# Kernel tuning notes

Measured on AMD Instinct MI355X. Metric: run time of the kernel, lower is better.

Reference implementation:

```python
import jax, jax.numpy as jnp
import numpy as np

B, NUM_SLOTS, D, TOP_K = 2048, 128, 1024, 8
DH = D // 2  # route_mlp hidden


def setup_inputs() -> dict:
    key = jax.random.key(0)
    ks = jax.random.split(key, 16)
    s = 0.02
    return {
        "x": jax.random.normal(ks[0], (B, D), jnp.float32),
        "S": jax.random.normal(ks[1], (B, NUM_SLOTS, D), jnp.float32),
        # route_mlp: Linear(2D, D//2) -> GELU -> Linear(D//2, NUM_SLOTS)
        "w1": jax.random.normal(ks[2], (DH, 2 * D), jnp.float32) * s,
        "b1": jnp.zeros((DH,), jnp.float32),
        "w2": jax.random.normal(ks[3], (NUM_SLOTS, DH), jnp.float32) * s,
        "b2": jnp.zeros((NUM_SLOTS,), jnp.float32),
        # GRUCell(D, D): torch layout, gates ordered (r, z, n)
        "gru_wih": jax.random.normal(ks[4], (3 * D, D), jnp.float32) * s,
        "gru_whh": jax.random.normal(ks[5], (3 * D, D), jnp.float32) * s,
        "gru_bih": jnp.zeros((3 * D,), jnp.float32),
        "gru_bhh": jnp.zeros((3 * D,), jnp.float32),
        "wval": jax.random.normal(ks[6], (D, D), jnp.float32) * s,
        "bval": jnp.zeros((D,), jnp.float32),
        "wout": jax.random.normal(ks[7], (D, D), jnp.float32) * s,
        "bout": jnp.zeros((D,), jnp.float32),
        "tau": jnp.ones((1,), jnp.float32),
    }


def reference(x, S, w1, b1, w2, b2, gru_wih, gru_whh, gru_bih, gru_bhh,
              wval, bval, wout, bout, tau):
    # Routing: context = [x, mean over slots]
    slot_mean = S.mean(axis=1)                                  # [B, D]
    ctx = jnp.concatenate([x, slot_mean], axis=-1)              # [B, 2D]
    h = jax.nn.gelu(ctx @ w1.T + b1, approximate=False)         # [B, DH]
    route_logits = (h @ w2.T + b2) / (jnp.abs(tau) + 0.1)       # [B, NUM_SLOTS]

    topk_vals, topk_idx = jax.lax.top_k(route_logits, TOP_K)    # [B, K]
    topk_w = jax.nn.softmax(topk_vals, axis=-1)                 # [B, K]

    # Gather selected slot states
    slot_states = jnp.take_along_axis(S, topk_idx[:, :, None], axis=1)  # [B, K, D]

    # GRUCell (torch semantics). Input part shared across the K slots.
    gi = x @ gru_wih.T + gru_bih                                # [B, 3D]
    gh = slot_states @ gru_whh.T + gru_bhh                      # [B, K, 3D]
    gi_r, gi_z, gi_n = jnp.split(gi, 3, axis=-1)
    gh_r, gh_z, gh_n = jnp.split(gh, 3, axis=-1)
    r = jax.nn.sigmoid(gi_r[:, None, :] + gh_r)
    z = jax.nn.sigmoid(gi_z[:, None, :] + gh_z)
    n = jnp.tanh(gi_n[:, None, :] + r * gh_n)
    updated = (1.0 - z) * n + z * slot_states                   # [B, K, D]

    # Scatter updated states back into slot memory
    S_new = S.at[jnp.arange(B)[:, None], topk_idx].set(updated)

    # Weighted value readout
    values = updated @ wval.T + bval                            # [B, K, D]
    mixed = jnp.einsum('bkd,bk->bd', values, topk_w)            # [B, D]
    output = mixed @ wout.T + bout                              # [B, D]
    return output, S_new
```

## Files before the change

kernel.cpp:

```cpp
#include <hip/hip_runtime.h>
#include <math.h>
#include <stdint.h>

#define B_   2048
#define NS_  128
#define D_   1024
#define K_   8
#define DH_  512
#define G3_  3072

typedef unsigned short u16;
typedef short bf16x8 __attribute__((ext_vector_type(8)));
typedef float f32x4 __attribute__((ext_vector_type(4)));

__device__ __forceinline__ float bf2f(u16 u) {
  union { unsigned i; float f; } v; v.i = ((unsigned)u) << 16; return v.f;
}
__device__ __forceinline__ u16 f2bf(float f) {
  unsigned x = __float_as_uint(f);
  return (u16)((x + 0x7fffu + ((x >> 16) & 1u)) >> 16);
}

#define AS1C(p) ((const __attribute__((address_space(1))) void*)(uintptr_t)(p))
#define AS3(p)  ((__attribute__((address_space(3))) void*)(unsigned)(uintptr_t)(p))

template<int DO_COPY>
__global__ __launch_bounds__(256)
void sp_copymean(const float* __restrict__ S, float* __restrict__ Snew,
                 float* __restrict__ mean) {
  const int b = blockIdx.x;
  const int t = threadIdx.x, d0 = t * 4;
  const f32x4* src = (const f32x4*)(S + (size_t)b * NS_ * D_) + t;
  f32x4* dst = (f32x4*)(Snew + (size_t)b * NS_ * D_) + t;
  double a0 = 0, a1 = 0, a2 = 0, a3 = 0;
  #pragma unroll 4
  for (int s = 0; s < NS_; ++s) {
    f32x4 v = __builtin_nontemporal_load(src);
    if (DO_COPY) __builtin_nontemporal_store(v, dst);
    a0 += v[0]; a1 += v[1]; a2 += v[2]; a3 += v[3];
    src += 256; dst += 256;
  }
  float4 m;
  m.x = (float)(a0 * (1.0 / 128.0)); m.y = (float)(a1 * (1.0 / 128.0));
  m.z = (float)(a2 * (1.0 / 128.0)); m.w = (float)(a3 * (1.0 / 128.0));
  *(float4*)&mean[(size_t)b * D_ + d0] = m;
}

__global__ __launch_bounds__(256)
void sp_convert_all(const float* __restrict__ x, const float* __restrict__ wih,
                    const float* __restrict__ whh, const float* __restrict__ wval,
                    const float* __restrict__ wout,
                    u16* __restrict__ xb, u16* __restrict__ wihb,
                    u16* __restrict__ whhb, u16* __restrict__ wvalb,
                    u16* __restrict__ woutb) {
  const int stride = gridDim.x * 256;
  for (int i = blockIdx.x * 256 + threadIdx.x; i < 2621440; i += stride) {
    const float* s; u16* d; int off;
    if (i < 524288)       { s = x;    d = xb;    off = i; }
    else if (i < 1310720) { s = wih;  d = wihb;  off = i - 524288; }
    else if (i < 2097152) { s = whh;  d = whhb;  off = i - 1310720; }
    else if (i < 2359296) { s = wval; d = wvalb; off = i - 2097152; }
    else                  { s = wout; d = woutb; off = i - 2359296; }
    float4 v = ((const float4*)s)[off];
    ushort4 o;
    o.x = f2bf(v.x); o.y = f2bf(v.y); o.z = f2bf(v.z); o.w = f2bf(v.w);
    ((ushort4*)d)[off] = o;
  }
}

__global__ __launch_bounds__(256)
void sp_gemm1(const float* __restrict__ x, const float* __restrict__ mean,
              const float* __restrict__ w1, const float* __restrict__ bias1,
              float* __restrict__ h) {
  __shared__ float As[16][68];
  __shared__ float Bs[16][36];
  int wg = blockIdx.x;
  wg = (wg & 7) * 64 + (wg >> 3);
  const int n0 = (wg & 15) * 32;
  const int m0 = (wg >> 4) * 64;
  const int t = threadIdx.x;
  const int tx = t & 15, ty = t >> 4;
  float acc[4][2] = {};
  const int sr = t >> 2, sc = (t & 3) * 4;
  for (int k0 = 0; k0 < 2 * D_; k0 += 16) {
    const float* src = (k0 < D_) ? (x + k0) : (mean + (k0 - D_));
    float4 va = *(const float4*)&src[(size_t)(m0 + sr) * D_ + sc];
    As[sc + 0][sr] = va.x; As[sc + 1][sr] = va.y; As[sc + 2][sr] = va.z; As[sc + 3][sr] = va.w;
    if (t < 128) {
      const int bn = t >> 2, bc = (t & 3) * 4;
      float4 vb = *(const float4*)&w1[(size_t)(n0 + bn) * (2 * D_) + k0 + bc];
      Bs[bc + 0][bn] = vb.x; Bs[bc + 1][bn] = vb.y; Bs[bc + 2][bn] = vb.z; Bs[bc + 3][bn] = vb.w;
    }
    __syncthreads();
    #pragma unroll
    for (int kk = 0; kk < 16; ++kk) {
      float4 a = *(const float4*)&As[kk][ty * 4];
      float2 bb = *(const float2*)&Bs[kk][tx * 2];
      acc[0][0] = fmaf(a.x, bb.x, acc[0][0]); acc[0][1] = fmaf(a.x, bb.y, acc[0][1]);
      acc[1][0] = fmaf(a.y, bb.x, acc[1][0]); acc[1][1] = fmaf(a.y, bb.y, acc[1][1]);
      acc[2][0] = fmaf(a.z, bb.x, acc[2][0]); acc[2][1] = fmaf(a.z, bb.y, acc[2][1]);
      acc[3][0] = fmaf(a.w, bb.x, acc[3][0]); acc[3][1] = fmaf(a.w, bb.y, acc[3][1]);
    }
    __syncthreads();
  }
  #pragma unroll
  for (int i = 0; i < 4; ++i) {
    #pragma unroll
    for (int j = 0; j < 2; ++j) {
      const int r = m0 + ty * 4 + i, c = n0 + tx * 2 + j;
      float v = acc[i][j] + bias1[c];
      v = 0.5f * v * (1.0f + erff(v * 0.70710678118654752f));
      h[(size_t)r * DH_ + c] = v;
    }
  }
}

__global__ __launch_bounds__(64)
void sp_route_topk(const float* __restrict__ h, const float* __restrict__ w2,
                   const float* __restrict__ b2, const float* __restrict__ tau,
                   int* __restrict__ tki, float* __restrict__ tkw) {
  __shared__ float hs[DH_];
  const int b = blockIdx.x, l = threadIdx.x;
  *(float4*)&hs[l * 4] = *(const float4*)&h[(size_t)b * DH_ + l * 4];
  *(float4*)&hs[256 + l * 4] = *(const float4*)&h[(size_t)b * DH_ + 256 + l * 4];
  __syncthreads();
  const double invd = 1.0 / ((double)fabsf(tau[0]) + 0.1);
  float v[2]; int id[2];
  #pragma unroll
  for (int c = 0; c < 2; ++c) {
    const int n = c * 64 + l;
    const float* wr = &w2[(size_t)n * DH_];
    double s = 0.0;
    for (int j = 0; j < DH_; j += 4) {
      float4 w4 = *(const float4*)&wr[j];
      s += (double)hs[j] * (double)w4.x;
      s += (double)hs[j + 1] * (double)w4.y;
      s += (double)hs[j + 2] * (double)w4.z;
      s += (double)hs[j + 3] * (double)w4.w;
    }
    v[c] = (float)((s + (double)b2[n]) * invd);
    id[c] = n;
  }
  float m0f = 0.f, sum = 0.f, mye = 0.f; int myi = 0;
  for (int r = 0; r < 8; ++r) {
    float mv; int mi;
    if (v[1] > v[0]) { mv = v[1]; mi = id[1]; } else { mv = v[0]; mi = id[0]; }
    #pragma unroll
    for (int off = 32; off > 0; off >>= 1) {
      float ov = __shfl_xor(mv, off);
      int oi = __shfl_xor(mi, off);
      if (ov > mv || (ov == mv && oi < mi)) { mv = ov; mi = oi; }
    }
    if (r == 0) m0f = mv;
    float er = expf(mv - m0f);
    sum += er;
    if (l == r) { mye = er; myi = mi; }
    if (mi == id[0]) v[0] = -3.0e38f;
    if (mi == id[1]) v[1] = -3.0e38f;
  }
  if (l < 8) { tki[b * K_ + l] = myi; tkw[b * K_ + l] = mye / sum; }
}

__global__ __launch_bounds__(256)
void sp_gather(const float* __restrict__ S, const int* __restrict__ tki,
               u16* __restrict__ slotb) {
  const int blk = blockIdx.x;
  const int b = blk >> 3, k = blk & 7;
  const int s = tki[b * K_ + k];
  const int t = threadIdx.x;
  float4 v = *(const float4*)&S[((size_t)b * NS_ + s) * D_ + t * 4];
  ushort4 o;
  o.x = f2bf(v.x); o.y = f2bf(v.y); o.z = f2bf(v.z); o.w = f2bf(v.w);
  *(ushort4*)&slotb[((size_t)b * K_ + k) * D_ + t * 4] = o;
}

template<int EPI>
__global__ __launch_bounds__(256)
void sp_gemm_bf16(const u16* __restrict__ A, const u16* __restrict__ Bm,
                  void* __restrict__ Cv, const float* __restrict__ bias,
                  int M, int N, int Kd, int nbx) {
  __shared__ u16 lA[128 * 32];
  __shared__ u16 lB[128 * 32];
  int wg = blockIdx.x;
  {
    const int nwg = nbx * ((M + 127) >> 7);
    const int cpx = nwg >> 3;
    wg = (wg & 7) * cpx + (wg >> 3);
  }
  const int m0 = (wg / nbx) * 128, n0 = (wg % nbx) * 128;
  const int t = threadIdx.x;
  const int lane = t & 63;
  const int w = t >> 6;
  const int wm = w >> 1, wn = w & 1;

  f32x4 acc[4][4] = {};

  const int srow = t >> 2;
  const int scol = (t & 3) * 8;
  const u16* gA0 = A + (size_t)(m0 + srow) * Kd + scol;
  const u16* gA1 = A + (size_t)(m0 + 64 + srow) * Kd + scol;
  const u16* gB0 = Bm + (size_t)(n0 + srow) * Kd + scol;
  const u16* gB1 = Bm + (size_t)(n0 + 64 + srow) * Kd + scol;
  u16* lAw = &lA[(t & 192) * 8];
  u16* lBw = &lB[(t & 192) * 8];

  const int kb = (lane >> 4) * 8;
  const int rA = wm * 64 + (lane & 15);
  const int rB = wn * 64 + (lane & 15);

  for (int k0 = 0; k0 < Kd; k0 += 32) {
    __builtin_amdgcn_global_load_lds(AS1C(gA0 + k0), AS3(lAw), 16, 0, 0);
    __builtin_amdgcn_global_load_lds(AS1C(gA1 + k0), AS3(lAw + 2048), 16, 0, 0);
    __builtin_amdgcn_global_load_lds(AS1C(gB0 + k0), AS3(lBw), 16, 0, 0);
    __builtin_amdgcn_global_load_lds(AS1C(gB1 + k0), AS3(lBw + 2048), 16, 0, 0);
    __syncthreads();
    bf16x8 af[4], bfr[4];
    #pragma unroll
    for (int fm = 0; fm < 4; ++fm)
      af[fm] = *(const bf16x8*)&lA[(rA + fm * 16) * 32 + kb];
    #pragma unroll
    for (int fn = 0; fn < 4; ++fn)
      bfr[fn] = *(const bf16x8*)&lB[(rB + fn * 16) * 32 + kb];
    #pragma unroll
    for (int fm = 0; fm < 4; ++fm) {
      #pragma unroll
      for (int fn = 0; fn < 4; ++fn)
        acc[fm][fn] = __builtin_amdgcn_mfma_f32_16x16x32_bf16(af[fm], bfr[fn], acc[fm][fn], 0, 0, 0);
    }
    __syncthreads();
  }

  #pragma unroll
  for (int fm = 0; fm < 4; ++fm) {
    #pragma unroll
    for (int fn = 0; fn < 4; ++fn) {
      #pragma unroll
      for (int i = 0; i < 4; ++i) {
        const int r = m0 + wm * 64 + fm * 16 + (lane >> 4) * 4 + i;
        const int c = n0 + wn * 64 + fn * 16 + (lane & 15);
        float v = acc[fm][fn][i];
        if constexpr (EPI >= 2) v += bias[c];
        if constexpr (EPI == 0 || EPI == 2)
          ((float*)Cv)[(size_t)r * N + c] = v;
        else
          ((u16*)Cv)[(size_t)r * N + c] = f2bf(v);
      }
    }
  }
}

template<bool DIRECT>
__global__ __launch_bounds__(256)
void sp_gh_gru(const u16* __restrict__ slotb, const u16* __restrict__ whhb,
               const float* __restrict__ gi, const float* __restrict__ bih,
               const float* __restrict__ bhh, const int* __restrict__ tki,
               const float* __restrict__ tkw, float* __restrict__ dst,
               u16* __restrict__ umixb) {
  __shared__ u16 lA[64 * 32];
  __shared__ u16 lB[192 * 32];
  __shared__ int   sTki[64];
  __shared__ float sTkw[64];
  int wg = blockIdx.x;
  wg = (wg & 7) * 512 + (wg >> 3);
  const int mt = wg >> 4, db = wg & 15;
  const int m0 = mt * 64, d0 = db * 64;
  const int t = threadIdx.x;
  const int lane = t & 63, w = t >> 6;
  const int wm = w >> 1, wn = w & 1;
  const int lane15 = lane & 15, hi = lane >> 4;

  if (t < 64) { sTki[t] = tki[m0 + t]; sTkw[t] = tkw[m0 + t]; }

  f32x4 acc[2][6] = {};

  const int srow = t >> 2;
  const int scol = (t & 3) * 8;
  const u16* gA  = slotb + (size_t)(m0 + srow) * D_ + scol;
  const u16* gB0 = whhb + (size_t)(d0 + srow) * D_ + scol;
  const u16* gB1 = whhb + (size_t)(D_ + d0 + srow) * D_ + scol;
  const u16* gB2 = whhb + (size_t)(2 * D_ + d0 + srow) * D_ + scol;
  u16* lAw  = &lA[(t & 192) * 8];
  u16* lBw0 = &lB[(t & 192) * 8];

  const int kb = hi * 8;
  const int rA = wm * 32 + lane15;
  const int rB = wn * 32 + lane15;

  for (int k0 = 0; k0 < D_; k0 += 32) {
    __builtin_amdgcn_global_load_lds(AS1C(gA  + k0), AS3(lAw), 16, 0, 0);
    __builtin_amdgcn_global_load_lds(AS1C(gB0 + k0), AS3(lBw0), 16, 0, 0);
    __builtin_amdgcn_global_load_lds(AS1C(gB1 + k0), AS3(lBw0 + 2048), 16, 0, 0);
    __builtin_amdgcn_global_load_lds(AS1C(gB2 + k0), AS3(lBw0 + 4096), 16, 0, 0);
    __syncthreads();
    bf16x8 af[2], bfr[6];
    #pragma unroll
    for (int fm = 0; fm < 2; ++fm)
      af[fm] = *(const bf16x8*)&lA[(rA + fm * 16) * 32 + kb];
    #pragma unroll
    for (int g = 0; g < 3; ++g) {
      #pragma unroll
      for (int f = 0; f < 2; ++f)
        bfr[g * 2 + f] = *(const bf16x8*)&lB[(g * 64 + rB + f * 16) * 32 + kb];
    }
    #pragma unroll
    for (int fm = 0; fm < 2; ++fm) {
      #pragma unroll
      for (int fn = 0; fn < 6; ++fn)
        acc[fm][fn] = __builtin_amdgcn_mfma_f32_16x16x32_bf16(af[fm], bfr[fn], acc[fm][fn], 0, 0, 0);
    }
    __syncthreads();
  }

  #pragma unroll
  for (int fm = 0; fm < 2; ++fm) {
    const int rbase = wm * 32 + fm * 16 + hi * 4;
    const int bglob = (m0 + rbase) >> 3;
    #pragma unroll
    for (int f = 0; f < 2; ++f) {
      const int dg = d0 + wn * 32 + f * 16 + lane15;
      const float Gr = gi[(size_t)bglob * G3_ + dg]           + bih[dg];
      const float Gz = gi[(size_t)bglob * G3_ + D_ + dg]      + bih[D_ + dg];
      const float Gn = gi[(size_t)bglob * G3_ + 2 * D_ + dg]  + bih[2 * D_ + dg];
      const float Br = bhh[dg], Bz = bhh[D_ + dg], Bn = bhh[2 * D_ + dg];
      float part = 0.f;
      #pragma unroll
      for (int i = 0; i < 4; ++i) {
        const int row = rbase + i;
        const int grow = m0 + row;
        const float slot = bf2f(slotb[(size_t)grow * D_ + dg]);
        const float rr = acc[fm][f][i] + Br;
        const float zz = acc[fm][f + 2][i] + Bz;
        const float nn = acc[fm][f + 4][i] + Bn;
        const float rg = 1.f / (1.f + expf(-(Gr + rr)));
        const float zg = 1.f / (1.f + expf(-(Gz + zz)));
        const float ng = tanhf(Gn + rg * nn);
        const float uv = (1.f - zg) * ng + zg * slot;
        part = fmaf(sTkw[row], uv, part);
        if (DIRECT)
          dst[((size_t)bglob * NS_ + sTki[row]) * D_ + dg] = uv;
        else
          dst[(size_t)grow * D_ + dg] = uv;
      }
      part += __shfl_xor(part, 16);
      if ((hi & 1) == 0)
        umixb[(size_t)bglob * D_ + dg] = f2bf(part);
    }
  }
}

__global__ __launch_bounds__(256)
void sp_copy_scatter(const float* __restrict__ S, const float* __restrict__ upd,
                     const int* __restrict__ tki, float* __restrict__ Snew) {
  const int b = blockIdx.x, t = threadIdx.x;
  const int d0 = t * 4;
  int idx[K_];
  #pragma unroll
  for (int k = 0; k < K_; ++k) idx[k] = tki[b * K_ + k];
  for (int s = 0; s < NS_; ++s) {
    int sk = -1;
    #pragma unroll
    for (int k = 0; k < K_; ++k) if (idx[k] == s) sk = k;
    float4 v;
    if (sk >= 0) v = *(const float4*)&upd[((size_t)b * K_ + sk) * D_ + d0];
    else         v = *(const float4*)&S[((size_t)b * NS_ + s) * D_ + d0];
    *(float4*)&Snew[((size_t)b * NS_ + s) * D_ + d0] = v;
  }
}

extern "C" void kernel_launch(void* const* d_in, const int* in_sizes, int n_in,
                              void* d_out, int out_size, void* d_ws, size_t ws_size,
                              hipStream_t stream) {
  const float* x    = (const float*)d_in[0];
  const float* S    = (const float*)d_in[1];
  const float* w1   = (const float*)d_in[2];
  const float* b1   = (const float*)d_in[3];
  const float* w2   = (const float*)d_in[4];
  const float* b2   = (const float*)d_in[5];
  const float* wih  = (const float*)d_in[6];
  const float* whh  = (const float*)d_in[7];
  const float* bih  = (const float*)d_in[8];
  const float* bhh  = (const float*)d_in[9];
  const float* wval = (const float*)d_in[10];
  const float* bval = (const float*)d_in[11];
  const float* wout = (const float*)d_in[12];
  const float* bout = (const float*)d_in[13];
  const float* tau  = (const float*)d_in[14];

  float* out  = (float*)d_out;
  float* Snew = out + (size_t)B_ * D_;

  const bool bigws = ws_size >= (size_t)400 * 1024 * 1024;
  char* bigbase = bigws ? (char*)d_ws : (char*)Snew;
  size_t bo = 0;
  auto balloc = [&](size_t bytes) -> void* {
    void* p = bigbase + bo; bo += (bytes + 255) & ~(size_t)255; return p;
  };

  float* mean  = (float*)balloc((size_t)B_ * D_ * 4);
  float* h     = (float*)balloc((size_t)B_ * DH_ * 4);
  u16* xb      = (u16*)balloc((size_t)B_ * D_ * 2);
  u16* wihb    = (u16*)balloc((size_t)G3_ * D_ * 2);
  u16* whhb    = (u16*)balloc((size_t)G3_ * D_ * 2);
  u16* wvalb   = (u16*)balloc((size_t)D_ * D_ * 2);
  u16* woutb   = (u16*)balloc((size_t)D_ * D_ * 2);
  float* gi    = (float*)balloc((size_t)B_ * G3_ * 4);
  u16* slotb   = (u16*)balloc((size_t)B_ * K_ * D_ * 2);
  u16* umixb   = (u16*)balloc((size_t)B_ * D_ * 2);
  u16* mixedb  = (u16*)balloc((size_t)B_ * D_ * 2);

  char* wsb = (char*)d_ws;
  size_t so = bigws ? bo : 0;
  auto salloc = [&](size_t bytes) -> void* {
    void* p = wsb + so; so += (bytes + 255) & ~(size_t)255; return p;
  };
  int*   tki = (int*)salloc((size_t)B_ * K_ * 4);
  float* tkw = (float*)salloc((size_t)B_ * K_ * 4);
  float* upd = bigws ? nullptr : (float*)salloc((size_t)B_ * K_ * D_ * 4);

  if (bigws) sp_copymean<1><<<B_, 256, 0, stream>>>(S, Snew, mean);
  else       sp_copymean<0><<<B_, 256, 0, stream>>>(S, Snew, mean);

  sp_convert_all<<<1024, 256, 0, stream>>>(x, wih, whh, wval, wout,
                                           xb, wihb, whhb, wvalb, woutb);

  sp_gemm1<<<512, 256, 0, stream>>>(x, mean, w1, b1, h);
  sp_route_topk<<<B_, 64, 0, stream>>>(h, w2, b2, tau, tki, tkw);

  sp_gather<<<B_ * K_, 256, 0, stream>>>(S, tki, slotb);

  sp_gemm_bf16<0><<<384, 256, 0, stream>>>(xb, wihb, gi, nullptr, B_, G3_, D_, G3_ / 128);

  if (bigws)
    sp_gh_gru<true><<<4096, 256, 0, stream>>>(slotb, whhb, gi, bih, bhh,
                                              tki, tkw, Snew, umixb);
  else
    sp_gh_gru<false><<<4096, 256, 0, stream>>>(slotb, whhb, gi, bih, bhh,
                                               tki, tkw, upd, umixb);

  sp_gemm_bf16<3><<<128, 256, 0, stream>>>(umixb, wvalb, mixedb, bval, B_, D_, D_, D_ / 128);
  sp_gemm_bf16<2><<<128, 256, 0, stream>>>(mixedb, woutb, out, bout, B_, D_, D_, D_ / 128);

  if (!bigws)
    sp_copy_scatter<<<B_, 256, 0, stream>>>(S, upd, tki, Snew);
}
```

Measured before the change: 866.3 us.

## Fold value and output projections into one weight, enlarge GRU tile, bf16 gi

Precomputes Wout·Wval as a single combined matrix (via a transposed bf16 wval and a small GEMM) plus a fused bias, so the final readout becomes one GEMM instead of two. The input-gate GEMM now writes bf16 instead of fp32, halving that intermediate's traffic. The gh/GRU kernel's M tile doubles to 128 rows with launch bounds raised to two blocks per CU, for more reuse of the whh tiles. The costs are an extra weight-fusion GEMM and transpose on every call, more rounding from bf16 gi and the product weight, and higher register pressure in the GRU kernel.

```diff
diff --git a/kernel.cpp b/kernel.cpp
--- a/kernel.cpp
+++ b/kernel.cpp
@@ -48,24 +48,67 @@
 
 __global__ __launch_bounds__(256)
 void sp_convert_all(const float* __restrict__ x, const float* __restrict__ wih,
-                    const float* __restrict__ whh, const float* __restrict__ wval,
-                    const float* __restrict__ wout,
+                    const float* __restrict__ whh, const float* __restrict__ wout,
                     u16* __restrict__ xb, u16* __restrict__ wihb,
-                    u16* __restrict__ whhb, u16* __restrict__ wvalb,
-                    u16* __restrict__ woutb) {
+                    u16* __restrict__ whhb, u16* __restrict__ woutb) {
   const int stride = gridDim.x * 256;
-  for (int i = blockIdx.x * 256 + threadIdx.x; i < 2621440; i += stride) {
+  for (int i = blockIdx.x * 256 + threadIdx.x; i < 2359296; i += stride) {
     const float* s; u16* d; int off;
     if (i < 524288)       { s = x;    d = xb;    off = i; }
     else if (i < 1310720) { s = wih;  d = wihb;  off = i - 524288; }
     else if (i < 2097152) { s = whh;  d = whhb;  off = i - 1310720; }
-    else if (i < 2359296) { s = wval; d = wvalb; off = i - 2097152; }
-    else                  { s = wout; d = woutb; off = i - 2359296; }
+    else                  { s = wout; d = woutb; off = i - 2097152; }
     float4 v = ((const float4*)s)[off];
     ushort4 o;
     o.x = f2bf(v.x); o.y = f2bf(v.y); o.z = f2bf(v.z); o.w = f2bf(v.w);
     ((ushort4*)d)[off] = o;
   }
+}
+
+__global__ __launch_bounds__(256)
+void sp_transpose_wval(const float* __restrict__ wval, u16* __restrict__ wvalT) {
+  __shared__ u16 tile[64][65];
+  const int bx = blockIdx.x & 15, by = blockIdx.x >> 4;
+  const int t = threadIdx.x;
+  const int r = t >> 4, c4 = (t & 15) * 4;
+  #pragma unroll
+  for (int p = 0; p < 4; ++p) {
+    const int row = by * 64 + p * 16 + r;
+    float4 v = *(const float4*)&wval[(size_t)row * D_ + bx * 64 + c4];
+    tile[p * 16 + r][c4 + 0] = f2bf(v.x);
+    tile[p * 16 + r][c4 + 1] = f2bf(v.y);
+    tile[p * 16 + r][c4 + 2] = f2bf(v.z);
+    tile[p * 16 + r][c4 + 3] = f2bf(v.w);
+  }
+  __syncthreads();
+  #pragma unroll
+  for (int p = 0; p < 4; ++p) {
+    const int jr = p * 16 + r;
+    ushort4 o;
+    o.x = tile[c4 + 0][jr];
+    o.y = tile[c4 + 1][jr];
+    o.z = tile[c4 + 2][jr];
+    o.w = tile[c4 + 3][jr];
+    *(ushort4*)&wvalT[(size_t)(bx * 64 + jr) * D_ + by * 64 + c4] = o;
+  }
+}
+
+__global__ __launch_bounds__(64)
+void sp_brow(const float* __restrict__ wout, const float* __restrict__ bval,
+             const float* __restrict__ bout, float* __restrict__ brow) {
+  const int i = blockIdx.x, l = threadIdx.x;
+  float s = 0.f;
+  const float* wr = &wout[(size_t)i * D_ + l * 16];
+  const float* bv = &bval[l * 16];
+  #pragma unroll
+  for (int j = 0; j < 16; j += 4) {
+    float4 w4 = *(const float4*)&wr[j];
+    float4 b4 = *(const float4*)&bv[j];
+    s += w4.x * b4.x + w4.y * b4.y + w4.z * b4.z + w4.w * b4.w;
+  }
+  #pragma unroll
+  for (int off = 32; off > 0; off >>= 1) s += __shfl_xor(s, off);
+  if (l == 0) brow[i] = s + bout[i];
 }
 
 __global__ __launch_bounds__(256)
@@ -250,51 +293,53 @@
 }
 
 template<bool DIRECT>
-__global__ __launch_bounds__(256)
+__global__ __launch_bounds__(256, 2)
 void sp_gh_gru(const u16* __restrict__ slotb, const u16* __restrict__ whhb,
-               const float* __restrict__ gi, const float* __restrict__ bih,
+               const u16* __restrict__ gib, const float* __restrict__ bih,
                const float* __restrict__ bhh, const int* __restrict__ tki,
                const float* __restrict__ tkw, float* __restrict__ dst,
                u16* __restrict__ umixb) {
-  __shared__ u16 lA[64 * 32];
+  __shared__ u16 lA[128 * 32];
   __shared__ u16 lB[192 * 32];
-  __shared__ int   sTki[64];
-  __shared__ float sTkw[64];
+  __shared__ int   sTki[128];
+  __shared__ float sTkw[128];
   int wg = blockIdx.x;
-  wg = (wg & 7) * 512 + (wg >> 3);
+  wg = (wg & 7) * 256 + (wg >> 3);
   const int mt = wg >> 4, db = wg & 15;
-  const int m0 = mt * 64, d0 = db * 64;
+  const int m0 = mt * 128, d0 = db * 64;
   const int t = threadIdx.x;
   const int lane = t & 63, w = t >> 6;
   const int wm = w >> 1, wn = w & 1;
   const int lane15 = lane & 15, hi = lane >> 4;
 
-  if (t < 64) { sTki[t] = tki[m0 + t]; sTkw[t] = tkw[m0 + t]; }
-
-  f32x4 acc[2][6] = {};
+  if (t < 128) { sTki[t] = tki[m0 + t]; sTkw[t] = tkw[m0 + t]; }
+
+  f32x4 acc[4][6] = {};
 
   const int srow = t >> 2;
   const int scol = (t & 3) * 8;
-  const u16* gA  = slotb + (size_t)(m0 + srow) * D_ + scol;
+  const u16* gA0 = slotb + (size_t)(m0 + srow) * D_ + scol;
+  const u16* gA1 = slotb + (size_t)(m0 + 64 + srow) * D_ + scol;
   const u16* gB0 = whhb + (size_t)(d0 + srow) * D_ + scol;
   const u16* gB1 = whhb + (size_t)(D_ + d0 + srow) * D_ + scol;
   const u16* gB2 = whhb + (size_t)(2 * D_ + d0 + srow) * D_ + scol;
-  u16* lAw  = &lA[(t & 192) * 8];
-  u16* lBw0 = &lB[(t & 192) * 8];
+  u16* lAw = &lA[(t & 192) * 8];
+  u16* lBw = &lB[(t & 192) * 8];
 
   const int kb = hi * 8;
-  const int rA = wm * 32 + lane15;
+  const int rA = wm * 64 + lane15;
   const int rB = wn * 32 + lane15;
 
   for (int k0 = 0; k0 < D_; k0 += 32) {
-    __builtin_amdgcn_global_load_lds(AS1C(gA  + k0), AS3(lAw), 16, 0, 0);
-    __builtin_amdgcn_global_load_lds(AS1C(gB0 + k0), AS3(lBw0), 16, 0, 0);
-    __builtin_amdgcn_global_load_lds(AS1C(gB1 + k0), AS3(lBw0 + 2048), 16, 0, 0);
-    __builtin_amdgcn_global_load_lds(AS1C(gB2 + k0), AS3(lBw0 + 4096), 16, 0, 0);
-    __syncthreads();
-    bf16x8 af[2], bfr[6];
-    #pragma unroll
-    for (int fm = 0; fm < 2; ++fm)
+    __builtin_amdgcn_global_load_lds(AS1C(gA0 + k0), AS3(lAw), 16, 0, 0);
+    __builtin_amdgcn_global_load_lds(AS1C(gA1 + k0), AS3(lAw + 2048), 16, 0, 0);
+    __builtin_amdgcn_global_load_lds(AS1C(gB0 + k0), AS3(lBw), 16, 0, 0);
+    __builtin_amdgcn_global_load_lds(AS1C(gB1 + k0), AS3(lBw + 2048), 16, 0, 0);
+    __builtin_amdgcn_global_load_lds(AS1C(gB2 + k0), AS3(lBw + 4096), 16, 0, 0);
+    __syncthreads();
+    bf16x8 af[4], bfr[6];
+    #pragma unroll
+    for (int fm = 0; fm < 4; ++fm)
       af[fm] = *(const bf16x8*)&lA[(rA + fm * 16) * 32 + kb];
     #pragma unroll
     for (int g = 0; g < 3; ++g) {
@@ -303,7 +348,7 @@
         bfr[g * 2 + f] = *(const bf16x8*)&lB[(g * 64 + rB + f * 16) * 32 + kb];
     }
     #pragma unroll
-    for (int fm = 0; fm < 2; ++fm) {
+    for (int fm = 0; fm < 4; ++fm) {
       #pragma unroll
       for (int fn = 0; fn < 6; ++fn)
         acc[fm][fn] = __builtin_amdgcn_mfma_f32_16x16x32_bf16(af[fm], bfr[fn], acc[fm][fn], 0, 0, 0);
@@ -312,15 +357,15 @@
   }
 
   #pragma unroll
-  for (int fm = 0; fm < 2; ++fm) {
-    const int rbase = wm * 32 + fm * 16 + hi * 4;
+  for (int fm = 0; fm < 4; ++fm) {
+    const int rbase = wm * 64 + fm * 16 + hi * 4;
     const int bglob = (m0 + rbase) >> 3;
     #pragma unroll
     for (int f = 0; f < 2; ++f) {
       const int dg = d0 + wn * 32 + f * 16 + lane15;
-      const float Gr = gi[(size_t)bglob * G3_ + dg]           + bih[dg];
-      const float Gz = gi[(size_t)bglob * G3_ + D_ + dg]      + bih[D_ + dg];
-      const float Gn = gi[(size_t)bglob * G3_ + 2 * D_ + dg]  + bih[2 * D_ + dg];
+      const float Gr = bf2f(gib[(size_t)bglob * G3_ + dg])          + bih[dg];
+      const float Gz = bf2f(gib[(size_t)bglob * G3_ + D_ + dg])     + bih[D_ + dg];
+      const float Gn = bf2f(gib[(size_t)bglob * G3_ + 2 * D_ + dg]) + bih[2 * D_ + dg];
       const float Br = bhh[dg], Bz = bhh[D_ + dg], Bn = bhh[2 * D_ + dg];
       float part = 0.f;
       #pragma unroll
@@ -401,12 +446,13 @@
   u16* xb      = (u16*)balloc((size_t)B_ * D_ * 2);
   u16* wihb    = (u16*)balloc((size_t)G3_ * D_ * 2);
   u16* whhb    = (u16*)balloc((size_t)G3_ * D_ * 2);
-  u16* wvalb   = (u16*)balloc((size_t)D_ * D_ * 2);
   u16* woutb   = (u16*)balloc((size_t)D_ * D_ * 2);
-  float* gi    = (float*)balloc((size_t)B_ * G3_ * 4);
+  u16* wvalTb  = (u16*)balloc((size_t)D_ * D_ * 2);
+  u16* Wrob    = (u16*)balloc((size_t)D_ * D_ * 2);
+  u16* gib     = (u16*)balloc((size_t)B_ * G3_ * 2);
   u16* slotb   = (u16*)balloc((size_t)B_ * K_ * D_ * 2);
   u16* umixb   = (u16*)balloc((size_t)B_ * D_ * 2);
-  u16* mixedb  = (u16*)balloc((size_t)B_ * D_ * 2);
+  float* brow  = (float*)balloc((size_t)D_ * 4);
 
   char* wsb = (char*)d_ws;
   size_t so = bigws ? bo : 0;
@@ -420,25 +466,27 @@
   if (bigws) sp_copymean<1><<<B_, 256, 0, stream>>>(S, Snew, mean);
   else       sp_copymean<0><<<B_, 256, 0, stream>>>(S, Snew, mean);
 
-  sp_convert_all<<<1024, 256, 0, stream>>>(x, wih, whh, wval, wout,
-                                           xb, wihb, whhb, wvalb, woutb);
+  sp_convert_all<<<1024, 256, 0, stream>>>(x, wih, whh, wout, xb, wihb, whhb, woutb);
+  sp_transpose_wval<<<256, 256, 0, stream>>>(wval, wvalTb);
+
+  sp_gemm_bf16<1><<<64, 256, 0, stream>>>(woutb, wvalTb, Wrob, nullptr, D_, D_, D_, 8);
+  sp_brow<<<D_, 64, 0, stream>>>(wout, bval, bout, brow);
 
   sp_gemm1<<<512, 256, 0, stream>>>(x, mean, w1, b1, h);
   sp_route_topk<<<B_, 64, 0, stream>>>(h, w2, b2, tau, tki, tkw);
 
   sp_gather<<<B_ * K_, 256, 0, stream>>>(S, tki, slotb);
 
-  sp_gemm_bf16<0><<<384, 256, 0, stream>>>(xb, wihb, gi, nullptr, B_, G3_, D_, G3_ / 128);
+  sp_gemm_bf16<1><<<384, 256, 0, stream>>>(xb, wihb, gib, nullptr, B_, G3_, D_, G3_ / 128);
 
   if (bigws)
-    sp_gh_gru<true><<<4096, 256, 0, stream>>>(slotb, whhb, gi, bih, bhh,
+    sp_gh_gru<true><<<2048, 256, 0, stream>>>(slotb, whhb, gib, bih, bhh,
                                               tki, tkw, Snew, umixb);
   else
-    sp_gh_gru<false><<<4096, 256, 0, stream>>>(slotb, whhb, gi, bih, bhh,
+    sp_gh_gru<false><<<2048, 256, 0, stream>>>(slotb, whhb, gib, bih, bhh,
                                                tki, tkw, upd, umixb);
 
-  sp_gemm_bf16<3><<<128, 256, 0, stream>>>(umixb, wvalb, mixedb, bval, B_, D_, D_, D_ / 128);
-  sp_gemm_bf16<2><<<128, 256, 0, stream>>>(mixedb, woutb, out, bout, B_, D_, D_, D_ / 128);
+  sp_gemm_bf16<2><<<128, 256, 0, stream>>>(umixb, Wrob, out, brow, B_, D_, D_, 8);
 
   if (!bigws)
     sp_copy_scatter<<<B_, 256, 0, stream>>>(S, upd, tki, Snew);
```

Measured after the change: 835.3 us. -3.6%, faster.
